# Kernel optimization log

Hardware: AMD Instinct MI355X
Metric: run time of the kernel (lower is better)

## Reference

```python
import jax, jax.numpy as jnp
import numpy as np

WINDOW_SIZE = 7
CHANNELS = 3
C1 = 0.01 ** 2
C2 = 0.03 ** 2


def _gaussian_window():
    # 1D gaussian, sigma=1.5, normalized; outer product -> 2D window
    coords = jnp.arange(WINDOW_SIZE, dtype=jnp.float32) - WINDOW_SIZE // 2
    g = jnp.exp(-coords ** 2 / (2 * 1.5 ** 2))
    g = g / g.sum()
    w2d = g[:, None] * g[None, :]  # [7,7]
    # depthwise kernel [C,1,7,7] (OIHW with feature_group_count=C)
    return jnp.tile(w2d[None, None], (CHANNELS, 1, 1, 1))


def _dwconv(x, window):
    pad = WINDOW_SIZE // 2
    return jax.lax.conv_general_dilated(
        x, window,
        window_strides=(1, 1),
        padding=[(pad, pad), (pad, pad)],
        dimension_numbers=('NCHW', 'OIHW', 'NCHW'),
        feature_group_count=CHANNELS,
    )


def setup_inputs() -> dict:
    key = jax.random.key(0)
    k1, k2 = jax.random.split(key)
    shape = (16, 3, 512, 512)
    enhanced = jax.random.uniform(k1, shape, dtype=jnp.float32)
    target = jax.random.uniform(k2, shape, dtype=jnp.float32)
    return {"enhanced": enhanced, "target": target}


def reference(enhanced, target):
    window = _gaussian_window()
    mu1 = _dwconv(enhanced, window)
    mu2 = _dwconv(target, window)
    mu1_sq = mu1 ** 2
    mu2_sq = mu2 ** 2
    mu1_mu2 = mu1 * mu2
    sigma1_sq = _dwconv(enhanced ** 2, window) - mu1_sq
    sigma2_sq = _dwconv(target ** 2, window) - mu2_sq
    sigma12 = _dwconv(enhanced * target, window) - mu1_mu2
    ssim_map = ((2 * mu1_mu2 + C1) * (2 * sigma12 + C2)) / (
        (mu1_sq + mu2_sq + C1) * (sigma1_sq + sigma2_sq + C2))
    return 1.0 - ssim_map.mean()
```

## Files before the change

kernel.cpp:

```cpp
#include <hip/hip_runtime.h>


#define MT 16
#define HALO 3
#define IN_H 22
#define SLOTS 17
#define IMG_H 512
#define IMG_W 512
#define NPLANES 48
#define SSIM_C1 1.0e-4f
#define SSIM_C2 9.0e-4f

static __device__ constexpr float G[7] = {
    0.03663284536f, 0.11128076166f, 0.21674531251f, 0.27068216094f,
    0.21674531251f, 0.11128076166f, 0.03663284536f};

__device__ __forceinline__ float2 pk_fma(const float2 a, const float2 b,
                                         const float2 c) {
  float2 d;
  asm("v_pk_fma_f32 %0, %1, %2, %3" : "=v"(d) : "v"(a), "v"(b), "v"(c));
  return d;
}

__device__ __forceinline__ float4 ld4z(const float* __restrict__ row, int col) {
  if (col >= 0 && col + 3 < IMG_W) {
    return *reinterpret_cast<const float4*>(row + col);
  }
  float4 v;
  v.x = ((unsigned)(col + 0) < IMG_W) ? row[col + 0] : 0.f;
  v.y = ((unsigned)(col + 1) < IMG_W) ? row[col + 1] : 0.f;
  v.z = ((unsigned)(col + 2) < IMG_W) ? row[col + 2] : 0.f;
  v.w = ((unsigned)(col + 3) < IMG_W) ? row[col + 3] : 0.f;
  return v;
}

__global__ __launch_bounds__(256, 4) void ssim_wave_kernel(
    const float* __restrict__ x, const float* __restrict__ y,
    float* __restrict__ partial) {
  __shared__ __align__(16) float4 hbuf[4][IN_H][SLOTS];
  __shared__ float wsum[4];

  const int tid = threadIdx.x;
  const int wid = tid >> 6;
  const int lane = tid & 63;
  const int tx = blockIdx.x * 4 + wid;
  const int ty = blockIdx.y;
  const int plane = blockIdx.z;
  const float* __restrict__ xp = x + (size_t)plane * (IMG_H * IMG_W);
  const float* __restrict__ yp = y + (size_t)plane * (IMG_H * IMG_W);
  const int x0 = tx * MT;
  const int y0 = ty * MT - HALO;
  const bool edge = (tx == 0) | (tx == 31) | (ty == 0) | (ty == 31);
  float4(*mybuf)[SLOTS] = hbuf[wid];

  if (lane < IN_H * 2) {
    const int r = lane >> 1;
    const int cg = lane & 1;
    const int gy = y0 + r;
    const int bcol = x0 + 8 * cg - 4;
    float4 xv0, xv1, xv2, xv3, yv0, yv1, yv2, yv3;
    if (!edge) {
      const float* xr = xp + (size_t)gy * IMG_W + bcol;
      const float* yr = yp + (size_t)gy * IMG_W + bcol;
      xv0 = *reinterpret_cast<const float4*>(xr);
      xv1 = *reinterpret_cast<const float4*>(xr + 4);
      xv2 = *reinterpret_cast<const float4*>(xr + 8);
      xv3 = *reinterpret_cast<const float4*>(xr + 12);
      yv0 = *reinterpret_cast<const float4*>(yr);
      yv1 = *reinterpret_cast<const float4*>(yr + 4);
      yv2 = *reinterpret_cast<const float4*>(yr + 8);
      yv3 = *reinterpret_cast<const float4*>(yr + 12);
    } else if ((unsigned)gy < IMG_H) {
      const float* xr = xp + (size_t)gy * IMG_W;
      const float* yr = yp + (size_t)gy * IMG_W;
      xv0 = ld4z(xr, bcol);
      xv1 = ld4z(xr, bcol + 4);
      xv2 = ld4z(xr, bcol + 8);
      xv3 = ld4z(xr, bcol + 12);
      yv0 = ld4z(yr, bcol);
      yv1 = ld4z(yr, bcol + 4);
      yv2 = ld4z(yr, bcol + 8);
      yv3 = ld4z(yr, bcol + 12);
    } else {
      const float4 z = make_float4(0.f, 0.f, 0.f, 0.f);
      xv0 = xv1 = xv2 = xv3 = z;
      yv0 = yv1 = yv2 = yv3 = z;
    }
    const float wx[16] = {xv0.x, xv0.y, xv0.z, xv0.w, xv1.x, xv1.y, xv1.z,
                          xv1.w, xv2.x, xv2.y, xv2.z, xv2.w, xv3.x, xv3.y,
                          xv3.z, xv3.w};
    const float wy[16] = {yv0.x, yv0.y, yv0.z, yv0.w, yv1.x, yv1.y, yv1.z,
                          yv1.w, yv2.x, yv2.y, yv2.z, yv2.w, yv3.x, yv3.y,
                          yv3.z, yv3.w};
    float2 A[8], B[8];
#pragma unroll
    for (int j = 0; j < 8; ++j) {
      A[j] = make_float2(0.f, 0.f);
      B[j] = make_float2(0.f, 0.f);
    }
#pragma unroll
    for (int wi = 1; wi < 15; ++wi) {
      const float xv = wx[wi];
      const float yv = wy[wi];
      const float2 xyp = make_float2(xv, yv);
      const float2 spp = make_float2(fmaf(xv, xv, yv * yv), xv * yv);
#pragma unroll
      for (int j = 0; j < 8; ++j) {
        const int k = wi - 1 - j;
        if (k >= 0 && k < 7) {
          const float2 gk2 = make_float2(G[k], G[k]);
          A[j] = pk_fma(gk2, xyp, A[j]);
          B[j] = pk_fma(gk2, spp, B[j]);
        }
      }
    }
#pragma unroll
    for (int j = 0; j < 8; ++j) {
      mybuf[r][8 * cg + j] = make_float4(A[j].x, A[j].y, B[j].x, B[j].y);
    }
  }

  __builtin_amdgcn_sched_barrier(0);
  asm volatile("s_waitcnt lgkmcnt(0)" ::: "memory");
  __builtin_amdgcn_sched_barrier(0);

  const int c = lane & 15;
  const int rg = lane >> 4;
  float2 M[4], S4[4];
#pragma unroll
  for (int t = 0; t < 4; ++t) {
    M[t] = make_float2(0.f, 0.f);
    S4[t] = make_float2(0.f, 0.f);
  }
#pragma unroll
  for (int j = 0; j < 10; ++j) {
    const float4 v = mybuf[4 * rg + j][c];
    const float2 mv = make_float2(v.x, v.y);
    const float2 sv = make_float2(v.z, v.w);
#pragma unroll
    for (int t = 0; t < 4; ++t) {
      const int k = j - t;
      if (k >= 0 && k < 7) {
        const float2 gk2 = make_float2(G[k], G[k]);
        M[t] = pk_fma(gk2, mv, M[t]);
        S4[t] = pk_fma(gk2, sv, S4[t]);
      }
    }
  }
  float acc = 0.f;
#pragma unroll
  for (int t = 0; t < 4; ++t) {
    const float mu1 = M[t].x, mu2 = M[t].y;
    const float mu12 = mu1 * mu2;
    const float msq = fmaf(mu1, mu1, mu2 * mu2);
    const float sig12 = S4[t].y - mu12;
    const float sigsum = S4[t].x - msq;
    const float num = fmaf(2.f, mu12, SSIM_C1) * fmaf(2.f, sig12, SSIM_C2);
    const float den = (msq + SSIM_C1) * (sigsum + SSIM_C2);
    float r = __builtin_amdgcn_rcpf(den);
    r = r * fmaf(-den, r, 2.f);
    acc = fmaf(num, r, acc);
  }

#pragma unroll
  for (int off = 32; off > 0; off >>= 1) acc += __shfl_down(acc, off, 64);
  if (lane == 0) wsum[wid] = acc;
  __syncthreads();
  if (tid == 0) {
    partial[((size_t)plane * 32 + ty) * 8 + blockIdx.x] =
        wsum[0] + wsum[1] + wsum[2] + wsum[3];
  }
}

__global__ __launch_bounds__(1024) void ssim_reduce_kernel(
    const float* __restrict__ partial, int n, float* __restrict__ out) {
  float acc = 0.f;
  const int nv = n >> 2;
  const float4* __restrict__ p4 = reinterpret_cast<const float4*>(partial);
  for (int i = threadIdx.x; i < nv; i += 1024) {
    const float4 v = p4[i];
    acc += (v.x + v.y) + (v.z + v.w);
  }
#pragma unroll
  for (int off = 32; off > 0; off >>= 1) acc += __shfl_down(acc, off, 64);
  __shared__ float wsum[16];
  if ((threadIdx.x & 63) == 0) wsum[threadIdx.x >> 6] = acc;
  __syncthreads();
  if (threadIdx.x == 0) {
    float s = 0.f;
#pragma unroll
    for (int w = 0; w < 16; ++w) s += wsum[w];
    out[0] = 1.f - s * (1.f / (float)(NPLANES * IMG_H * IMG_W));
  }
}

extern "C" void kernel_launch(void* const* d_in, const int* in_sizes, int n_in,
                              void* d_out, int out_size, void* d_ws, size_t ws_size,
                              hipStream_t stream) {
  const float* enhanced = (const float*)d_in[0];
  const float* target = (const float*)d_in[1];
  float* out = (float*)d_out;
  float* partial = (float*)d_ws;

  dim3 grid(8, 32, NPLANES);
  dim3 block(256, 1, 1);
  ssim_wave_kernel<<<grid, block, 0, stream>>>(enhanced, target, partial);

  const int nblocks = 8 * 32 * NPLANES;
  ssim_reduce_kernel<<<1, 1024, 0, stream>>>(partial, nblocks, out);
}
```

Baseline: 143.8 us.

## Chain four vertical tiles per wave with a ring buffer for halo rows

Each wave now walks down four consecutive 16x16 tiles instead of one, keeping horizontally filtered rows in a 32-row LDS ring buffer. The 6 halo rows are not reloaded or refiltered for each tile, which removes most of the redundant global loads and horizontal-pass work at tile boundaries. The grid shrinks by 4x in y and the partial-sum indexing changes to match. In exchange, the work inside each wave becomes serial, with less parallelism to hide memory latency, and only 32 lanes stay active in the later horizontal passes.

```diff
diff --git a/kernel.cpp b/kernel.cpp
--- a/kernel.cpp
+++ b/kernel.cpp
@@ -1,10 +1,9 @@
 #include <hip/hip_runtime.h>
 
 
-#define MT 16
 #define HALO 3
-#define IN_H 22
 #define SLOTS 17
+#define RING 32
 #define IMG_H 512
 #define IMG_W 512
 #define NPLANES 48
@@ -34,140 +33,152 @@
   return v;
 }
 
-__global__ __launch_bounds__(256, 4) void ssim_wave_kernel(
+__global__ __launch_bounds__(256, 4) void ssim_chain_kernel(
     const float* __restrict__ x, const float* __restrict__ y,
     float* __restrict__ partial) {
-  __shared__ __align__(16) float4 hbuf[4][IN_H][SLOTS];
+  __shared__ __align__(16) float4 ring[4][RING][SLOTS];
   __shared__ float wsum[4];
 
   const int tid = threadIdx.x;
   const int wid = tid >> 6;
   const int lane = tid & 63;
   const int tx = blockIdx.x * 4 + wid;
-  const int ty = blockIdx.y;
+  const int cy = blockIdx.y;
   const int plane = blockIdx.z;
   const float* __restrict__ xp = x + (size_t)plane * (IMG_H * IMG_W);
   const float* __restrict__ yp = y + (size_t)plane * (IMG_H * IMG_W);
-  const int x0 = tx * MT;
-  const int y0 = ty * MT - HALO;
-  const bool edge = (tx == 0) | (tx == 31) | (ty == 0) | (ty == 31);
-  float4(*mybuf)[SLOTS] = hbuf[wid];
-
-  if (lane < IN_H * 2) {
-    const int r = lane >> 1;
-    const int cg = lane & 1;
-    const int gy = y0 + r;
-    const int bcol = x0 + 8 * cg - 4;
-    float4 xv0, xv1, xv2, xv3, yv0, yv1, yv2, yv3;
-    if (!edge) {
-      const float* xr = xp + (size_t)gy * IMG_W + bcol;
-      const float* yr = yp + (size_t)gy * IMG_W + bcol;
-      xv0 = *reinterpret_cast<const float4*>(xr);
-      xv1 = *reinterpret_cast<const float4*>(xr + 4);
-      xv2 = *reinterpret_cast<const float4*>(xr + 8);
-      xv3 = *reinterpret_cast<const float4*>(xr + 12);
-      yv0 = *reinterpret_cast<const float4*>(yr);
-      yv1 = *reinterpret_cast<const float4*>(yr + 4);
-      yv2 = *reinterpret_cast<const float4*>(yr + 8);
-      yv3 = *reinterpret_cast<const float4*>(yr + 12);
-    } else if ((unsigned)gy < IMG_H) {
-      const float* xr = xp + (size_t)gy * IMG_W;
-      const float* yr = yp + (size_t)gy * IMG_W;
-      xv0 = ld4z(xr, bcol);
-      xv1 = ld4z(xr, bcol + 4);
-      xv2 = ld4z(xr, bcol + 8);
-      xv3 = ld4z(xr, bcol + 12);
-      yv0 = ld4z(yr, bcol);
-      yv1 = ld4z(yr, bcol + 4);
-      yv2 = ld4z(yr, bcol + 8);
-      yv3 = ld4z(yr, bcol + 12);
-    } else {
-      const float4 z = make_float4(0.f, 0.f, 0.f, 0.f);
-      xv0 = xv1 = xv2 = xv3 = z;
-      yv0 = yv1 = yv2 = yv3 = z;
-    }
-    const float wx[16] = {xv0.x, xv0.y, xv0.z, xv0.w, xv1.x, xv1.y, xv1.z,
-                          xv1.w, xv2.x, xv2.y, xv2.z, xv2.w, xv3.x, xv3.y,
-                          xv3.z, xv3.w};
-    const float wy[16] = {yv0.x, yv0.y, yv0.z, yv0.w, yv1.x, yv1.y, yv1.z,
-                          yv1.w, yv2.x, yv2.y, yv2.z, yv2.w, yv3.x, yv3.y,
-                          yv3.z, yv3.w};
-    float2 A[8], B[8];
-#pragma unroll
-    for (int j = 0; j < 8; ++j) {
-      A[j] = make_float2(0.f, 0.f);
-      B[j] = make_float2(0.f, 0.f);
-    }
-#pragma unroll
-    for (int wi = 1; wi < 15; ++wi) {
-      const float xv = wx[wi];
-      const float yv = wy[wi];
-      const float2 xyp = make_float2(xv, yv);
-      const float2 spp = make_float2(fmaf(xv, xv, yv * yv), xv * yv);
+  const int x0 = tx * 16;
+  const int yb = cy * 64;
+  const bool edge_x = (tx == 0) | (tx == 31);
+  float4(*rb)[SLOTS] = ring[wid];
+
+  auto h_rows = [&](int gr0, int nrows, bool edgey) {
+    if (lane < 2 * nrows) {
+      const int gy = gr0 + (lane >> 1);
+      const int cg = lane & 1;
+      const int bcol = x0 + 8 * cg - 4;
+      const bool edge = edge_x | edgey;
+      float4 xv0, xv1, xv2, xv3, yv0, yv1, yv2, yv3;
+      if (!edge) {
+        const float* xr = xp + (size_t)gy * IMG_W + bcol;
+        const float* yr = yp + (size_t)gy * IMG_W + bcol;
+        xv0 = *reinterpret_cast<const float4*>(xr);
+        xv1 = *reinterpret_cast<const float4*>(xr + 4);
+        xv2 = *reinterpret_cast<const float4*>(xr + 8);
+        xv3 = *reinterpret_cast<const float4*>(xr + 12);
+        yv0 = *reinterpret_cast<const float4*>(yr);
+        yv1 = *reinterpret_cast<const float4*>(yr + 4);
+        yv2 = *reinterpret_cast<const float4*>(yr + 8);
+        yv3 = *reinterpret_cast<const float4*>(yr + 12);
+      } else if ((unsigned)gy < IMG_H) {
+        const float* xr = xp + (size_t)gy * IMG_W;
+        const float* yr = yp + (size_t)gy * IMG_W;
+        xv0 = ld4z(xr, bcol);
+        xv1 = ld4z(xr, bcol + 4);
+        xv2 = ld4z(xr, bcol + 8);
+        xv3 = ld4z(xr, bcol + 12);
+        yv0 = ld4z(yr, bcol);
+        yv1 = ld4z(yr, bcol + 4);
+        yv2 = ld4z(yr, bcol + 8);
+        yv3 = ld4z(yr, bcol + 12);
+      } else {
+        const float4 z = make_float4(0.f, 0.f, 0.f, 0.f);
+        xv0 = xv1 = xv2 = xv3 = z;
+        yv0 = yv1 = yv2 = yv3 = z;
+      }
+      const float wx[16] = {xv0.x, xv0.y, xv0.z, xv0.w, xv1.x, xv1.y, xv1.z,
+                            xv1.w, xv2.x, xv2.y, xv2.z, xv2.w, xv3.x, xv3.y,
+                            xv3.z, xv3.w};
+      const float wy[16] = {yv0.x, yv0.y, yv0.z, yv0.w, yv1.x, yv1.y, yv1.z,
+                            yv1.w, yv2.x, yv2.y, yv2.z, yv2.w, yv3.x, yv3.y,
+                            yv3.z, yv3.w};
+      float2 A[8], B[8];
 #pragma unroll
       for (int j = 0; j < 8; ++j) {
-        const int k = wi - 1 - j;
+        A[j] = make_float2(0.f, 0.f);
+        B[j] = make_float2(0.f, 0.f);
+      }
+#pragma unroll
+      for (int wi = 1; wi < 15; ++wi) {
+        const float xv = wx[wi];
+        const float yv = wy[wi];
+        const float2 xyp = make_float2(xv, yv);
+        const float2 spp = make_float2(fmaf(xv, xv, yv * yv), xv * yv);
+#pragma unroll
+        for (int j = 0; j < 8; ++j) {
+          const int k = wi - 1 - j;
+          if (k >= 0 && k < 7) {
+            const float2 gk2 = make_float2(G[k], G[k]);
+            A[j] = pk_fma(gk2, xyp, A[j]);
+            B[j] = pk_fma(gk2, spp, B[j]);
+          }
+        }
+      }
+      const int rr = gy & (RING - 1);
+#pragma unroll
+      for (int j = 0; j < 8; ++j) {
+        rb[rr][8 * cg + j] = make_float4(A[j].x, A[j].y, B[j].x, B[j].y);
+      }
+    }
+  };
+
+  const int c = lane & 15;
+  const int rg = lane >> 4;
+  auto v_chunk = [&](int i) -> float {
+    float2 M[4], S4[4];
+#pragma unroll
+    for (int t = 0; t < 4; ++t) {
+      M[t] = make_float2(0.f, 0.f);
+      S4[t] = make_float2(0.f, 0.f);
+    }
+#pragma unroll
+    for (int j = 0; j < 10; ++j) {
+      const float4 v = rb[(16 * i + 4 * rg - 3 + j) & (RING - 1)][c];
+      const float2 mv = make_float2(v.x, v.y);
+      const float2 sv = make_float2(v.z, v.w);
+#pragma unroll
+      for (int t = 0; t < 4; ++t) {
+        const int k = j - t;
         if (k >= 0 && k < 7) {
           const float2 gk2 = make_float2(G[k], G[k]);
-          A[j] = pk_fma(gk2, xyp, A[j]);
-          B[j] = pk_fma(gk2, spp, B[j]);
+          M[t] = pk_fma(gk2, mv, M[t]);
+          S4[t] = pk_fma(gk2, sv, S4[t]);
         }
       }
     }
-#pragma unroll
-    for (int j = 0; j < 8; ++j) {
-      mybuf[r][8 * cg + j] = make_float4(A[j].x, A[j].y, B[j].x, B[j].y);
-    }
-  }
-
-  __builtin_amdgcn_sched_barrier(0);
-  asm volatile("s_waitcnt lgkmcnt(0)" ::: "memory");
-  __builtin_amdgcn_sched_barrier(0);
-
-  const int c = lane & 15;
-  const int rg = lane >> 4;
-  float2 M[4], S4[4];
-#pragma unroll
-  for (int t = 0; t < 4; ++t) {
-    M[t] = make_float2(0.f, 0.f);
-    S4[t] = make_float2(0.f, 0.f);
-  }
-#pragma unroll
-  for (int j = 0; j < 10; ++j) {
-    const float4 v = mybuf[4 * rg + j][c];
-    const float2 mv = make_float2(v.x, v.y);
-    const float2 sv = make_float2(v.z, v.w);
+    float a = 0.f;
 #pragma unroll
     for (int t = 0; t < 4; ++t) {
-      const int k = j - t;
-      if (k >= 0 && k < 7) {
-        const float2 gk2 = make_float2(G[k], G[k]);
-        M[t] = pk_fma(gk2, mv, M[t]);
-        S4[t] = pk_fma(gk2, sv, S4[t]);
-      }
-    }
-  }
+      const float mu1 = M[t].x, mu2 = M[t].y;
+      const float mu12 = mu1 * mu2;
+      const float msq = fmaf(mu1, mu1, mu2 * mu2);
+      const float sig12 = S4[t].y - mu12;
+      const float sigsum = S4[t].x - msq;
+      const float num = fmaf(2.f, mu12, SSIM_C1) * fmaf(2.f, sig12, SSIM_C2);
+      const float den = (msq + SSIM_C1) * (sigsum + SSIM_C2);
+      float r = __builtin_amdgcn_rcpf(den);
+      r = r * fmaf(-den, r, 2.f);
+      a = fmaf(num, r, a);
+    }
+    return a;
+  };
+
   float acc = 0.f;
-#pragma unroll
-  for (int t = 0; t < 4; ++t) {
-    const float mu1 = M[t].x, mu2 = M[t].y;
-    const float mu12 = mu1 * mu2;
-    const float msq = fmaf(mu1, mu1, mu2 * mu2);
-    const float sig12 = S4[t].y - mu12;
-    const float sigsum = S4[t].x - msq;
-    const float num = fmaf(2.f, mu12, SSIM_C1) * fmaf(2.f, sig12, SSIM_C2);
-    const float den = (msq + SSIM_C1) * (sigsum + SSIM_C2);
-    float r = __builtin_amdgcn_rcpf(den);
-    r = r * fmaf(-den, r, 2.f);
-    acc = fmaf(num, r, acc);
-  }
+  h_rows(yb - 3, 22, cy == 0);
+  acc += v_chunk(0);
+  h_rows(yb + 19, 16, false);
+  acc += v_chunk(1);
+  h_rows(yb + 35, 16, false);
+  acc += v_chunk(2);
+  h_rows(yb + 51, 16, cy == 7);
+  acc += v_chunk(3);
 
 #pragma unroll
   for (int off = 32; off > 0; off >>= 1) acc += __shfl_down(acc, off, 64);
   if (lane == 0) wsum[wid] = acc;
   __syncthreads();
   if (tid == 0) {
-    partial[((size_t)plane * 32 + ty) * 8 + blockIdx.x] =
+    partial[((size_t)plane * 8 + blockIdx.y) * 8 + blockIdx.x] =
         wsum[0] + wsum[1] + wsum[2] + wsum[3];
   }
 }
@@ -202,10 +213,10 @@
   float* out = (float*)d_out;
   float* partial = (float*)d_ws;
 
-  dim3 grid(8, 32, NPLANES);
+  dim3 grid(8, 8, NPLANES);
   dim3 block(256, 1, 1);
-  ssim_wave_kernel<<<grid, block, 0, stream>>>(enhanced, target, partial);
-
-  const int nblocks = 8 * 32 * NPLANES;
+  ssim_chain_kernel<<<grid, block, 0, stream>>>(enhanced, target, partial);
+
+  const int nblocks = 8 * 8 * NPLANES;
   ssim_reduce_kernel<<<1, 1024, 0, stream>>>(partial, nblocks, out);
 }
```

Result: no change. 144.6 us (+0.6%).
